# Performance work log

Hardware: AMD Instinct MI355X
Metric: run time of the kernel (lower is better)

## Reference

```python
import jax, jax.numpy as jnp
import numpy as np

B, S, D = 2, 2048, 2048
HQ, HKV, HD = 16, 4, 128
EPS = 1e-8


def _rope_tables(seq_len, dim, base=10000.0):
    inv_freq = 1.0 / (base ** (jnp.arange(0, dim, 2, dtype=jnp.float32) / dim))
    freqs = jnp.outer(jnp.arange(seq_len, dtype=jnp.float32), inv_freq)  # S x dim/2
    emb = jnp.concatenate([freqs, freqs], axis=-1)  # S x dim
    return jnp.cos(emb), jnp.sin(emb)


def setup_inputs() -> dict:
    key = jax.random.key(0)
    ks = jax.random.split(key, 6)
    cos_theta, sin_theta = _rope_tables(S, HD)
    return {
        "x": jax.random.normal(ks[0], (B, S, D), dtype=jnp.float32),
        "Wq": jax.random.normal(ks[1], (D, HQ * HD), dtype=jnp.float32) * 0.02,
        "Wk": jax.random.normal(ks[2], (D, HKV * HD), dtype=jnp.float32) * 0.02,
        "Wv": jax.random.normal(ks[3], (D, HKV * HD), dtype=jnp.float32) * 0.02,
        "Wo": jax.random.normal(ks[4], (HQ * HD, D), dtype=jnp.float32) * 0.02,
        "q_norm_w": jnp.zeros((HD,), dtype=jnp.float32),
        "k_norm_w": jnp.zeros((HD,), dtype=jnp.float32),
        "cos_theta": cos_theta,
        "sin_theta": sin_theta,
        "padding_mask": jnp.zeros((B, S), dtype=bool),
        "window_size": 1024,
    }


def _rmsnorm(x, w):
    return x * jax.lax.rsqrt(jnp.mean(x * x, axis=-1, keepdims=True) + EPS) * (1.0 + w)


def _rotate_half(x):
    x1, x2 = jnp.split(x, 2, axis=-1)
    return jnp.concatenate([-x2, x1], axis=-1)


def _rope(x, cos_t, sin_t):
    # x: B x H x S x d; cos/sin: S x d
    return x * cos_t[None, None] + _rotate_half(x) * sin_t[None, None]


def reference(x, Wq, Wk, Wv, Wo, q_norm_w, k_norm_w, cos_theta, sin_theta, padding_mask, window_size):
    b, s, _ = x.shape
    scale = HD ** -0.5
    q = (x @ Wq).reshape(b, s, HQ, HD).transpose(0, 2, 1, 3)   # b,HQ,s,d
    k = (x @ Wk).reshape(b, s, HKV, HD).transpose(0, 2, 1, 3)  # b,HKV,s,d
    v = (x @ Wv).reshape(b, s, HKV, HD).transpose(0, 2, 1, 3)
    q = _rope(_rmsnorm(q, q_norm_w), cos_theta[:s], sin_theta[:s])
    k = _rope(_rmsnorm(k, k_norm_w), cos_theta[:s], sin_theta[:s])

    # causal & sliding window & padding mask
    qi = jnp.arange(s)[:, None]
    ki = jnp.arange(s)[None, :]
    mask = (qi >= ki) & ((qi - ki) <= window_size)          # s x s
    pad = padding_mask[:, :, None] | padding_mask[:, None, :]  # b x s x s
    mask = mask[None] & ~pad                                 # b x s x s

    g = HQ // HKV
    qg = q.reshape(b, HKV, g, s, HD)
    scores = jnp.einsum('bngqd,bnkd->bngqk', qg, k) * scale  # b,HKV,g,s,s
    scores = jnp.where(mask[:, None, None], scores, -jnp.inf)
    attn = jax.nn.softmax(scores, axis=-1)
    out = jnp.einsum('bngqk,bnkd->bngqd', attn, v)
    out = out.reshape(b, HQ, s, HD).transpose(0, 2, 1, 3).reshape(b, s, HQ * HD)
    return out @ Wo
```

## Files before the change

### kernel.cpp

```cpp
#include <hip/hip_runtime.h>

typedef __attribute__((ext_vector_type(4))) float f32x4;
typedef __attribute__((ext_vector_type(8))) __bf16 bf16x8;
typedef __attribute__((ext_vector_type(4))) __bf16 bf16x4;

__device__ __forceinline__ void gload_lds16(const __bf16* g, __bf16* l) {
  __builtin_amdgcn_global_load_lds(
      (const __attribute__((address_space(1))) unsigned int*)(g),
      (__attribute__((address_space(3))) unsigned int*)(l), 16, 0, 0);
}

__global__ __launch_bounds__(256) void prep(
    const float* __restrict__ Wq, const float* __restrict__ Wk,
    const float* __restrict__ Wv, const float* __restrict__ Wo,
    const float4* __restrict__ x, const unsigned long long* __restrict__ pad,
    __bf16* __restrict__ Wqkvt, __bf16* __restrict__ Wot,
    bf16x4* __restrict__ xb, unsigned char* __restrict__ pad64) {
  const int bx = blockIdx.x, by = blockIdx.y;
  const int tx = threadIdx.x, ty = threadIdx.y;
  const int tid = ty * 32 + tx;
  if (bx >= 160) {
    int i = ((bx - 160) * 64 + by) * 256 + tid;
    float4 v = x[i];
    bf16x4 o = {(__bf16)v.x, (__bf16)v.y, (__bf16)v.z, (__bf16)v.w};
    xb[i] = o;
    return;
  }
  if (bx == 0 && by == 0 && tid < 64) {
    unsigned long long acc = 0;
#pragma unroll
    for (int i = 0; i < 8; ++i) acc |= pad[tid * 8 + i];
    pad64[tid] = (acc != 0) ? 1 : 0;
  }
  __shared__ float t[32][33];
  const float* src; __bf16* dst; int ss, c0;
  if (bx < 64)      { src = Wq; dst = Wqkvt;                       ss = 2048; c0 = bx * 32; }
  else if (bx < 80) { src = Wk; dst = Wqkvt + (size_t)2048 * 2048; ss = 512;  c0 = (bx - 64) * 32; }
  else if (bx < 96) { src = Wv; dst = Wqkvt + (size_t)2560 * 2048; ss = 512;  c0 = (bx - 80) * 32; }
  else              { src = Wo; dst = Wot;                         ss = 2048; c0 = (bx - 96) * 32; }
  const int r0 = by * 32;
#pragma unroll
  for (int i = ty; i < 32; i += 8)
    t[i][tx] = src[(size_t)(r0 + i) * ss + c0 + tx];
  __syncthreads();
#pragma unroll
  for (int i = ty; i < 32; i += 8)
    dst[(size_t)(c0 + i) * 2048 + r0 + tx] = (__bf16)t[tx][i];
}

__global__ __launch_bounds__(256) void gemm_qkv(
    const __bf16* __restrict__ A, const __bf16* __restrict__ Bt,
    __bf16* __restrict__ Qb, __bf16* __restrict__ Kb, __bf16* __restrict__ Vt) {
  __shared__ __align__(16) __bf16 smem[128 * 136];
  __bf16* As = smem;
  __bf16* Bs = smem + 128 * 32;
  __bf16* stage = smem;
  const int K = 2048;
  const int tid = threadIdx.x;
  const int lane = tid & 63;
  const int c15 = lane & 15, quad = lane >> 4;
  const int wm = ((tid >> 6) & 1) * 64;
  const int wn = (tid >> 7) * 64;
  const int jb = blockIdx.x;
  const int m0 = blockIdx.y * 128, n0 = jb * 128;
  const int wbase = tid & 192;

  f32x4 acc[4][4] = {};

  const int row0 = tid >> 2, cc0 = (tid & 3) * 8;
  const int row1 = (tid + 256) >> 2;
  const __bf16* a0 = A + (size_t)(m0 + row0) * K + cc0;
  const __bf16* a1 = A + (size_t)(m0 + row1) * K + cc0;
  const __bf16* b0 = Bt + (size_t)(n0 + row0) * K + cc0;
  const __bf16* b1 = Bt + (size_t)(n0 + row1) * K + cc0;
  __bf16* lA0 = As + (size_t)wbase * 8;
  __bf16* lA1 = As + (size_t)(256 + wbase) * 8;
  __bf16* lB0 = Bs + (size_t)wbase * 8;
  __bf16* lB1 = Bs + (size_t)(256 + wbase) * 8;

  for (int k0 = 0; k0 < K; k0 += 32) {
    gload_lds16(a0 + k0, lA0);
    gload_lds16(a1 + k0, lA1);
    gload_lds16(b0 + k0, lB0);
    gload_lds16(b1 + k0, lB1);
    __syncthreads();
    bf16x8 af[4], bfr[4];
#pragma unroll
    for (int i = 0; i < 4; ++i) {
      af[i]  = *(const bf16x8*)(As + (wm + i * 16 + c15) * 32 + quad * 8);
      bfr[i] = *(const bf16x8*)(Bs + (wn + i * 16 + c15) * 32 + quad * 8);
    }
#pragma unroll
    for (int i = 0; i < 4; ++i)
#pragma unroll
      for (int j = 0; j < 4; ++j)
        acc[i][j] = __builtin_amdgcn_mfma_f32_16x16x32_bf16(af[i], bfr[j], acc[i][j], 0, 0, 0);
    __syncthreads();
  }

  const int b = m0 >> 11;
  const int s0 = m0 & 2047;
  const int orow = tid >> 4, ocol = (tid & 15) * 8;

  if (jb >= 20) {
#pragma unroll
    for (int j = 0; j < 4; ++j) {
      int d = wn + j * 16 + c15;
#pragma unroll
      for (int i = 0; i < 4; ++i) {
        int sl = wm + i * 16 + quad * 4;
        bf16x4 o = {(__bf16)acc[i][j][0], (__bf16)acc[i][j][1],
                    (__bf16)acc[i][j][2], (__bf16)acc[i][j][3]};
        *(bf16x4*)(stage + (size_t)d * 136 + sl) = o;
      }
    }
    __syncthreads();
    __bf16* VtH = Vt + (((size_t)b * 4 + (jb - 20)) * 128) * 2048;
#pragma unroll
    for (int p = 0; p < 8; ++p) {
      int d = p * 16 + orow;
      *(bf16x8*)(VtH + (size_t)d * 2048 + s0 + ocol) =
          *(const bf16x8*)(stage + (size_t)d * 136 + ocol);
    }
    return;
  }

#pragma unroll
  for (int i = 0; i < 4; ++i)
#pragma unroll
    for (int j = 0; j < 4; ++j)
#pragma unroll
      for (int r = 0; r < 4; ++r)
        stage[(size_t)(wm + i * 16 + quad * 4 + r) * 136 + wn + j * 16 + c15] =
            (__bf16)acc[i][j][r];
  __syncthreads();
  __bf16* dstH = (jb < 16) ? Qb + (((size_t)b * 16 + jb) * 2048) * 128
                           : Kb + (((size_t)b * 4 + (jb - 16)) * 2048) * 128;
#pragma unroll
  for (int p = 0; p < 8; ++p) {
    int sl = p * 16 + orow;
    *(bf16x8*)(dstH + (size_t)(s0 + sl) * 128 + ocol) =
        *(const bf16x8*)(stage + (size_t)sl * 136 + ocol);
  }
}

__global__ __launch_bounds__(256) void norm_rope(
    __bf16* __restrict__ Qb, __bf16* __restrict__ Kb,
    const float* __restrict__ qw, const float* __restrict__ kw,
    const float* __restrict__ cosT, const float* __restrict__ sinT) {
  const int tid = threadIdx.x, w = tid >> 6, lane = tid & 63;
  const int v = blockIdx.x * 4 + w;
  const bool isQ = v < 65536;
  __bf16* base = isQ ? Qb + (size_t)v * 128 : Kb + (size_t)(v - 65536) * 128;
  const int s = v & 2047;
  float x1 = (float)base[lane], x2 = (float)base[lane + 64];
  float ss = x1 * x1 + x2 * x2;
#pragma unroll
  for (int d = 32; d; d >>= 1) ss += __shfl_xor(ss, d);
  float rn = rsqrtf(ss * (1.0f / 128.0f) + 1e-8f);
  const float* wt = isQ ? qw : kw;
  float n1 = x1 * rn * (1.0f + wt[lane]);
  float n2 = x2 * rn * (1.0f + wt[lane + 64]);
  float c1 = cosT[s * 128 + lane], c2 = cosT[s * 128 + 64 + lane];
  float s1 = sinT[s * 128 + lane], s2 = sinT[s * 128 + 64 + lane];
  const float QSC = 0.08838834764831845f * 1.4426950408889634f;
  float post = isQ ? QSC : 1.0f;
  base[lane]      = (__bf16)((n1 * c1 - n2 * s1) * post);
  base[lane + 64] = (__bf16)((n2 * c2 + n1 * s2) * post);
}

__global__ __launch_bounds__(256) void gemm_bt(const __bf16* __restrict__ A,
                                               const __bf16* __restrict__ Bt,
                                               float* __restrict__ C,
                                               int M, int N, int K) {
  __shared__ __align__(16) __bf16 As[128 * 32];
  __shared__ __align__(16) __bf16 Bs[128 * 32];
  const int tid = threadIdx.x;
  const int lane = tid & 63;
  const int c15 = lane & 15, quad = lane >> 4;
  const int wm = ((tid >> 6) & 1) * 64;
  const int wn = (tid >> 7) * 64;
  const int m0 = blockIdx.y * 128, n0 = blockIdx.x * 128;
  const int wbase = tid & 192;

  f32x4 acc[4][4] = {};

  const int row0 = tid >> 2, cc0 = (tid & 3) * 8;
  const int row1 = (tid + 256) >> 2;
  const __bf16* a0 = A + (size_t)(m0 + row0) * K + cc0;
  const __bf16* a1 = A + (size_t)(m0 + row1) * K + cc0;
  const __bf16* b0 = Bt + (size_t)(n0 + row0) * K + cc0;
  const __bf16* b1 = Bt + (size_t)(n0 + row1) * K + cc0;
  __bf16* lA0 = As + (size_t)wbase * 8;
  __bf16* lA1 = As + (size_t)(256 + wbase) * 8;
  __bf16* lB0 = Bs + (size_t)wbase * 8;
  __bf16* lB1 = Bs + (size_t)(256 + wbase) * 8;

  for (int k0 = 0; k0 < K; k0 += 32) {
    gload_lds16(a0 + k0, lA0);
    gload_lds16(a1 + k0, lA1);
    gload_lds16(b0 + k0, lB0);
    gload_lds16(b1 + k0, lB1);
    __syncthreads();
    bf16x8 af[4], bfr[4];
#pragma unroll
    for (int i = 0; i < 4; ++i) {
      af[i]  = *(const bf16x8*)(As + (wm + i * 16 + c15) * 32 + quad * 8);
      bfr[i] = *(const bf16x8*)(Bs + (wn + i * 16 + c15) * 32 + quad * 8);
    }
#pragma unroll
    for (int i = 0; i < 4; ++i)
#pragma unroll
      for (int j = 0; j < 4; ++j)
        acc[i][j] = __builtin_amdgcn_mfma_f32_16x16x32_bf16(af[i], bfr[j], acc[i][j], 0, 0, 0);
    __syncthreads();
  }

#pragma unroll
  for (int i = 0; i < 4; ++i) {
    int r0 = m0 + wm + i * 16 + quad * 4;
#pragma unroll
    for (int j = 0; j < 4; ++j) {
      int cc = n0 + wn + j * 16 + c15;
#pragma unroll
      for (int r = 0; r < 4; ++r)
        C[(size_t)(r0 + r) * N + cc] = acc[i][j][r];
    }
  }
}

__global__ __launch_bounds__(256) void attn(
    const __bf16* __restrict__ Qb, const __bf16* __restrict__ Kb,
    const __bf16* __restrict__ Vt, const unsigned char* __restrict__ pad,
    const unsigned char* __restrict__ pad64, const int* __restrict__ winp,
    __bf16* __restrict__ O) {
  const int S = 2048;
  __shared__ __align__(16) __bf16 Ks[64 * 128];
  __shared__ __align__(16) __bf16 Vs[128 * 64];
  __shared__ __align__(16) __bf16 Ps[4 * 16 * 72];
  const int tid = threadIdx.x, w = tid >> 6, lane = tid & 63;
  const int c15 = lane & 15, quad = lane >> 4;
  const int q0 = (gridDim.x - 1 - blockIdx.x) * 16;
  const int kv = blockIdx.y, b = blockIdx.z;
  const int h = kv * 4 + w;
  const int W = *winp;
  const unsigned char* padb = pad + (size_t)b * S;
  const unsigned char* pad64b = pad64 + b * 32;
  const __bf16* Qh = Qb + (((size_t)b * 16 + h) * S) * 128;
  const __bf16* Kh = Kb + (((size_t)b * 4 + kv) * S) * 128;
  const __bf16* Vh = Vt + (((size_t)b * 4 + kv) * 128) * (size_t)S;
  __bf16* Pw = Ps + w * 16 * 72;

  bf16x8 qf[4];
#pragma unroll
  for (int c = 0; c < 4; ++c)
    qf[c] = *(const bf16x8*)(Qh + (size_t)(q0 + c15) * 128 + c * 32 + quad * 8);

  f32x4 acc[8] = {};
  float lsum[4] = {0.f, 0.f, 0.f, 0.f};

  const int krow_i = lane >> 4, kch = lane & 15;
  const int vrow_i = lane >> 3, vch = lane & 7;

  int kb0 = q0 - W; if (kb0 < 0) kb0 = 0; kb0 &= ~63;

  for (int kb = kb0; kb <= q0 + 15; kb += 64) {
    __syncthreads();
#pragma unroll
    for (int i = 0; i < 4; ++i) {
      int row = w * 16 + i * 4 + krow_i;
      gload_lds16(Kh + (size_t)(kb + row) * 128 + ((kch ^ (row & 15)) * 8),
                  Ks + (w * 16 + i * 4) * 128);
    }
#pragma unroll
    for (int i = 0; i < 4; ++i) {
      int row = w * 32 + i * 8 + vrow_i;
      gload_lds16(Vh + (size_t)row * S + kb + ((vch ^ (row & 7)) * 8),
                  Vs + (w * 32 + i * 8) * 64);
    }
    __syncthreads();

    f32x4 sf[4];
#pragma unroll
    for (int nb = 0; nb < 4; ++nb) {
      f32x4 cacc = {};
#pragma unroll
      for (int c = 0; c < 4; ++c) {
        bf16x8 kf = *(const bf16x8*)(Ks + (nb * 16 + c15) * 128 + (((c * 4 + quad) ^ c15) * 8));
        cacc = __builtin_amdgcn_mfma_f32_16x16x32_bf16(qf[c], kf, cacc, 0, 0, 0);
      }
      sf[nb] = cacc;
    }

    const bool fast = (kb + 63 <= q0) && (q0 + 15 - kb <= W) && (pad64b[kb >> 6] == 0);
    if (fast) {
#pragma unroll
      for (int r = 0; r < 4; ++r) {
        float p0 = exp2f(sf[0][r]), p1 = exp2f(sf[1][r]);
        float p2 = exp2f(sf[2][r]), p3 = exp2f(sf[3][r]);
        lsum[r] += (p0 + p1) + (p2 + p3);
        int pr = (quad * 4 + r) * 72 + c15;
        Pw[pr] = (__bf16)p0; Pw[pr + 16] = (__bf16)p1;
        Pw[pr + 32] = (__bf16)p2; Pw[pr + 48] = (__bf16)p3;
      }
    } else {
#pragma unroll
      for (int r = 0; r < 4; ++r) {
        const int qi = q0 + quad * 4 + r;
        float p[4];
#pragma unroll
        for (int nb = 0; nb < 4; ++nb) {
          int ki = kb + nb * 16 + c15;
          bool ok = (ki <= qi) && ((qi - ki) <= W) && (padb[ki] == 0);
          float e = exp2f(sf[nb][r]);
          p[nb] = ok ? e : 0.0f;
        }
        lsum[r] += (p[0] + p[1]) + (p[2] + p[3]);
        int pr = (quad * 4 + r) * 72 + c15;
        Pw[pr] = (__bf16)p[0]; Pw[pr + 16] = (__bf16)p[1];
        Pw[pr + 32] = (__bf16)p[2]; Pw[pr + 48] = (__bf16)p[3];
      }
    }

    bf16x8 pf0 = *(const bf16x8*)(Pw + c15 * 72 + quad * 8);
    bf16x8 pf1 = *(const bf16x8*)(Pw + c15 * 72 + 32 + quad * 8);
#pragma unroll
    for (int nb = 0; nb < 8; ++nb) {
      int row = nb * 16 + c15;
      bf16x8 vf0 = *(const bf16x8*)(Vs + row * 64 + ((quad ^ (c15 & 7)) * 8));
      bf16x8 vf1 = *(const bf16x8*)(Vs + row * 64 + (((4 + quad) ^ (c15 & 7)) * 8));
      acc[nb] = __builtin_amdgcn_mfma_f32_16x16x32_bf16(pf0, vf0, acc[nb], 0, 0, 0);
      acc[nb] = __builtin_amdgcn_mfma_f32_16x16x32_bf16(pf1, vf1, acc[nb], 0, 0, 0);
    }
  }

#pragma unroll
  for (int r = 0; r < 4; ++r) {
    lsum[r] += __shfl_xor(lsum[r], 1);
    lsum[r] += __shfl_xor(lsum[r], 2);
    lsum[r] += __shfl_xor(lsum[r], 4);
    lsum[r] += __shfl_xor(lsum[r], 8);
  }
  float inv[4];
#pragma unroll
  for (int r = 0; r < 4; ++r) inv[r] = 1.0f / lsum[r];
#pragma unroll
  for (int nb = 0; nb < 8; ++nb)
#pragma unroll
    for (int r = 0; r < 4; ++r) {
      size_t idx = ((size_t)b * S + q0 + quad * 4 + r) * 2048 + h * 128 + nb * 16 + c15;
      O[idx] = (__bf16)(acc[nb][r] * inv[r]);
    }
}

extern "C" void kernel_launch(void* const* d_in, const int* in_sizes, int n_in,
                              void* d_out, int out_size, void* d_ws, size_t ws_size,
                              hipStream_t stream) {
  const float* x    = (const float*)d_in[0];
  const float* Wq   = (const float*)d_in[1];
  const float* Wk   = (const float*)d_in[2];
  const float* Wv   = (const float*)d_in[3];
  const float* Wo   = (const float*)d_in[4];
  const float* qw   = (const float*)d_in[5];
  const float* kw   = (const float*)d_in[6];
  const float* cosT = (const float*)d_in[7];
  const float* sinT = (const float*)d_in[8];
  const unsigned char* pad = (const unsigned char*)d_in[9];
  const int* win    = (const int*)d_in[10];

  char* ws = (char*)d_ws;
  __bf16* xb    = (__bf16*)(ws + 0);
  __bf16* Wqkvt = (__bf16*)(ws + 16777216);
  __bf16* Wot   = (__bf16*)(ws + 29360128);
  __bf16* Qb    = (__bf16*)(ws + 37748736);
  __bf16* Kb    = (__bf16*)(ws + 54525952);
  __bf16* Vt    = (__bf16*)(ws + 58720256);
  __bf16* Ob    = (__bf16*)(ws + 62914560);
  unsigned char* pad64 = (unsigned char*)(ws + 79691776);

  prep<<<dim3(288, 64, 1), dim3(32, 8, 1), 0, stream>>>(
      Wq, Wk, Wv, Wo, (const float4*)x, (const unsigned long long*)pad,
      Wqkvt, Wot, (bf16x4*)xb, pad64);

  gemm_qkv<<<dim3(24, 32, 1), 256, 0, stream>>>(xb, Wqkvt, Qb, Kb, Vt);

  norm_rope<<<20480, 256, 0, stream>>>(Qb, Kb, qw, kw, cosT, sinT);

  attn<<<dim3(128, 4, 2), 256, 0, stream>>>(Qb, Kb, Vt, pad, pad64, win, Ob);

  gemm_bt<<<dim3(16, 32, 1), 256, 0, stream>>>(Ob, Wot, (float*)d_out, 4096, 2048, 2048);
}
```

Before: 335.3 us.

## Process 32 query rows per wave in attention to reuse K/V tiles

Each wave in the attention kernel now handles two 16-row query sub-tiles instead of one. Every K and V fragment loaded from LDS feeds two MFMAs, and each block covers twice as many query rows, so the grid shrinks from 128 to 64 query blocks. The block order is also reversed for the second batch to balance causal work across the grid. In exchange, register pressure roughly doubles, which may lower occupancy, and fewer blocks means less parallelism across the GPU.

```diff
diff --git a/kernel.cpp b/kernel.cpp
--- a/kernel.cpp
+++ b/kernel.cpp
@@ -237,11 +237,13 @@
   const int S = 2048;
   __shared__ __align__(16) __bf16 Ks[64 * 128];
   __shared__ __align__(16) __bf16 Vs[128 * 64];
-  __shared__ __align__(16) __bf16 Ps[4 * 16 * 72];
+  __shared__ __align__(16) __bf16 Ps[4 * 32 * 72];
   const int tid = threadIdx.x, w = tid >> 6, lane = tid & 63;
   const int c15 = lane & 15, quad = lane >> 4;
-  const int q0 = (gridDim.x - 1 - blockIdx.x) * 16;
-  const int kv = blockIdx.y, b = blockIdx.z;
+  const int b = blockIdx.z;
+  const int bx = (b == 0) ? blockIdx.x : (gridDim.x - 1 - blockIdx.x);
+  const int q0 = ((int)gridDim.x - 1 - bx) * 32;
+  const int kv = blockIdx.y;
   const int h = kv * 4 + w;
   const int W = *winp;
   const unsigned char* padb = pad + (size_t)b * S;
@@ -249,22 +251,25 @@
   const __bf16* Qh = Qb + (((size_t)b * 16 + h) * S) * 128;
   const __bf16* Kh = Kb + (((size_t)b * 4 + kv) * S) * 128;
   const __bf16* Vh = Vt + (((size_t)b * 4 + kv) * 128) * (size_t)S;
-  __bf16* Pw = Ps + w * 16 * 72;
-
-  bf16x8 qf[4];
-#pragma unroll
-  for (int c = 0; c < 4; ++c)
-    qf[c] = *(const bf16x8*)(Qh + (size_t)(q0 + c15) * 128 + c * 32 + quad * 8);
-
-  f32x4 acc[8] = {};
-  float lsum[4] = {0.f, 0.f, 0.f, 0.f};
+  __bf16* Pw = Ps + w * 32 * 72;
+
+  bf16x8 qf0[4], qf1[4];
+#pragma unroll
+  for (int c = 0; c < 4; ++c) {
+    qf0[c] = *(const bf16x8*)(Qh + (size_t)(q0 + c15) * 128 + c * 32 + quad * 8);
+    qf1[c] = *(const bf16x8*)(Qh + (size_t)(q0 + 16 + c15) * 128 + c * 32 + quad * 8);
+  }
+
+  f32x4 acc0[8] = {}, acc1[8] = {};
+  float lsum0[4] = {0.f, 0.f, 0.f, 0.f};
+  float lsum1[4] = {0.f, 0.f, 0.f, 0.f};
 
   const int krow_i = lane >> 4, kch = lane & 15;
   const int vrow_i = lane >> 3, vch = lane & 7;
 
   int kb0 = q0 - W; if (kb0 < 0) kb0 = 0; kb0 &= ~63;
 
-  for (int kb = kb0; kb <= q0 + 15; kb += 64) {
+  for (int kb = kb0; kb <= q0 + 31; kb += 64) {
     __syncthreads();
 #pragma unroll
     for (int i = 0; i < 4; ++i) {
@@ -280,76 +285,101 @@
     }
     __syncthreads();
 
-    f32x4 sf[4];
+    f32x4 sf0[4], sf1[4];
 #pragma unroll
     for (int nb = 0; nb < 4; ++nb) {
-      f32x4 cacc = {};
+      f32x4 ca = {}, cb = {};
 #pragma unroll
       for (int c = 0; c < 4; ++c) {
         bf16x8 kf = *(const bf16x8*)(Ks + (nb * 16 + c15) * 128 + (((c * 4 + quad) ^ c15) * 8));
-        cacc = __builtin_amdgcn_mfma_f32_16x16x32_bf16(qf[c], kf, cacc, 0, 0, 0);
+        ca = __builtin_amdgcn_mfma_f32_16x16x32_bf16(qf0[c], kf, ca, 0, 0, 0);
+        cb = __builtin_amdgcn_mfma_f32_16x16x32_bf16(qf1[c], kf, cb, 0, 0, 0);
       }
-      sf[nb] = cacc;
-    }
-
-    const bool fast = (kb + 63 <= q0) && (q0 + 15 - kb <= W) && (pad64b[kb >> 6] == 0);
+      sf0[nb] = ca; sf1[nb] = cb;
+    }
+
+    const bool fast = (kb + 63 <= q0) && (q0 + 31 - kb <= W) && (pad64b[kb >> 6] == 0);
     if (fast) {
 #pragma unroll
       for (int r = 0; r < 4; ++r) {
-        float p0 = exp2f(sf[0][r]), p1 = exp2f(sf[1][r]);
-        float p2 = exp2f(sf[2][r]), p3 = exp2f(sf[3][r]);
-        lsum[r] += (p0 + p1) + (p2 + p3);
+        float a0 = exp2f(sf0[0][r]), a1 = exp2f(sf0[1][r]);
+        float a2 = exp2f(sf0[2][r]), a3 = exp2f(sf0[3][r]);
+        lsum0[r] += (a0 + a1) + (a2 + a3);
         int pr = (quad * 4 + r) * 72 + c15;
-        Pw[pr] = (__bf16)p0; Pw[pr + 16] = (__bf16)p1;
-        Pw[pr + 32] = (__bf16)p2; Pw[pr + 48] = (__bf16)p3;
+        Pw[pr] = (__bf16)a0; Pw[pr + 16] = (__bf16)a1;
+        Pw[pr + 32] = (__bf16)a2; Pw[pr + 48] = (__bf16)a3;
+        float b0 = exp2f(sf1[0][r]), b1 = exp2f(sf1[1][r]);
+        float b2 = exp2f(sf1[2][r]), b3 = exp2f(sf1[3][r]);
+        lsum1[r] += (b0 + b1) + (b2 + b3);
+        int qr = pr + 16 * 72;
+        Pw[qr] = (__bf16)b0; Pw[qr + 16] = (__bf16)b1;
+        Pw[qr + 32] = (__bf16)b2; Pw[qr + 48] = (__bf16)b3;
       }
     } else {
 #pragma unroll
       for (int r = 0; r < 4; ++r) {
-        const int qi = q0 + quad * 4 + r;
-        float p[4];
+        const int qi0 = q0 + quad * 4 + r;
+        const int qi1 = qi0 + 16;
+        float p0[4], p1[4];
 #pragma unroll
         for (int nb = 0; nb < 4; ++nb) {
           int ki = kb + nb * 16 + c15;
-          bool ok = (ki <= qi) && ((qi - ki) <= W) && (padb[ki] == 0);
-          float e = exp2f(sf[nb][r]);
-          p[nb] = ok ? e : 0.0f;
+          bool okp = (padb[ki] == 0);
+          bool ok0 = (ki <= qi0) && ((qi0 - ki) <= W) && okp;
+          bool ok1 = (ki <= qi1) && ((qi1 - ki) <= W) && okp;
+          float e0 = exp2f(sf0[nb][r]);
+          float e1 = exp2f(sf1[nb][r]);
+          p0[nb] = ok0 ? e0 : 0.0f;
+          p1[nb] = ok1 ? e1 : 0.0f;
         }
-        lsum[r] += (p[0] + p[1]) + (p[2] + p[3]);
+        lsum0[r] += (p0[0] + p0[1]) + (p0[2] + p0[3]);
+        lsum1[r] += (p1[0] + p1[1]) + (p1[2] + p1[3]);
         int pr = (quad * 4 + r) * 72 + c15;
-        Pw[pr] = (__bf16)p[0]; Pw[pr + 16] = (__bf16)p[1];
-        Pw[pr + 32] = (__bf16)p[2]; Pw[pr + 48] = (__bf16)p[3];
+        Pw[pr] = (__bf16)p0[0]; Pw[pr + 16] = (__bf16)p0[1];
+        Pw[pr + 32] = (__bf16)p0[2]; Pw[pr + 48] = (__bf16)p0[3];
+        int qr = pr + 16 * 72;
+        Pw[qr] = (__bf16)p1[0]; Pw[qr + 16] = (__bf16)p1[1];
+        Pw[qr + 32] = (__bf16)p1[2]; Pw[qr + 48] = (__bf16)p1[3];
       }
     }
 
-    bf16x8 pf0 = *(const bf16x8*)(Pw + c15 * 72 + quad * 8);
-    bf16x8 pf1 = *(const bf16x8*)(Pw + c15 * 72 + 32 + quad * 8);
+    bf16x8 pf00 = *(const bf16x8*)(Pw + c15 * 72 + quad * 8);
+    bf16x8 pf01 = *(const bf16x8*)(Pw + c15 * 72 + 32 + quad * 8);
+    bf16x8 pf10 = *(const bf16x8*)(Pw + (16 + c15) * 72 + quad * 8);
+    bf16x8 pf11 = *(const bf16x8*)(Pw + (16 + c15) * 72 + 32 + quad * 8);
 #pragma unroll
     for (int nb = 0; nb < 8; ++nb) {
       int row = nb * 16 + c15;
       bf16x8 vf0 = *(const bf16x8*)(Vs + row * 64 + ((quad ^ (c15 & 7)) * 8));
       bf16x8 vf1 = *(const bf16x8*)(Vs + row * 64 + (((4 + quad) ^ (c15 & 7)) * 8));
-      acc[nb] = __builtin_amdgcn_mfma_f32_16x16x32_bf16(pf0, vf0, acc[nb], 0, 0, 0);
-      acc[nb] = __builtin_amdgcn_mfma_f32_16x16x32_bf16(pf1, vf1, acc[nb], 0, 0, 0);
+      acc0[nb] = __builtin_amdgcn_mfma_f32_16x16x32_bf16(pf00, vf0, acc0[nb], 0, 0, 0);
+      acc0[nb] = __builtin_amdgcn_mfma_f32_16x16x32_bf16(pf01, vf1, acc0[nb], 0, 0, 0);
+      acc1[nb] = __builtin_amdgcn_mfma_f32_16x16x32_bf16(pf10, vf0, acc1[nb], 0, 0, 0);
+      acc1[nb] = __builtin_amdgcn_mfma_f32_16x16x32_bf16(pf11, vf1, acc1[nb], 0, 0, 0);
     }
   }
 
 #pragma unroll
   for (int r = 0; r < 4; ++r) {
-    lsum[r] += __shfl_xor(lsum[r], 1);
-    lsum[r] += __shfl_xor(lsum[r], 2);
-    lsum[r] += __shfl_xor(lsum[r], 4);
-    lsum[r] += __shfl_xor(lsum[r], 8);
-  }
-  float inv[4];
-#pragma unroll
-  for (int r = 0; r < 4; ++r) inv[r] = 1.0f / lsum[r];
+    lsum0[r] += __shfl_xor(lsum0[r], 1);
+    lsum0[r] += __shfl_xor(lsum0[r], 2);
+    lsum0[r] += __shfl_xor(lsum0[r], 4);
+    lsum0[r] += __shfl_xor(lsum0[r], 8);
+    lsum1[r] += __shfl_xor(lsum1[r], 1);
+    lsum1[r] += __shfl_xor(lsum1[r], 2);
+    lsum1[r] += __shfl_xor(lsum1[r], 4);
+    lsum1[r] += __shfl_xor(lsum1[r], 8);
+  }
+  float inv0[4], inv1[4];
+#pragma unroll
+  for (int r = 0; r < 4; ++r) { inv0[r] = 1.0f / lsum0[r]; inv1[r] = 1.0f / lsum1[r]; }
 #pragma unroll
   for (int nb = 0; nb < 8; ++nb)
 #pragma unroll
     for (int r = 0; r < 4; ++r) {
       size_t idx = ((size_t)b * S + q0 + quad * 4 + r) * 2048 + h * 128 + nb * 16 + c15;
-      O[idx] = (__bf16)(acc[nb][r] * inv[r]);
+      O[idx] = (__bf16)(acc0[nb][r] * inv0[r]);
+      O[idx + (size_t)16 * 2048] = (__bf16)(acc1[nb][r] * inv1[r]);
     }
 }
 
@@ -386,7 +416,7 @@
 
   norm_rope<<<20480, 256, 0, stream>>>(Qb, Kb, qw, kw, cosT, sinT);
 
-  attn<<<dim3(128, 4, 2), 256, 0, stream>>>(Qb, Kb, Vt, pad, pad64, win, Ob);
+  attn<<<dim3(64, 4, 2), 256, 0, stream>>>(Qb, Kb, Vt, pad, pad64, win, Ob);
 
   gemm_bt<<<dim3(16, 32, 1), 256, 0, stream>>>(Ob, Wot, (float*)d_out, 4096, 2048, 2048);
 }
```

Measured after the change: 322.5 us. -3.8%, faster.
